# Kernel optimization log

Measured on AMD Instinct MI355X. Metric: run time of the kernel, lower is better.

## Reference

```python
import jax, jax.numpy as jnp
import numpy as np

MARGIN = 0.5


def _pairwise_sqdist(a, b):
    # ||a_i - b_j||^2 = |a_i|^2 + |b_j|^2 - 2 a_i . b_j  -> [N, N]
    a2 = jnp.sum(a * a, axis=1)
    b2 = jnp.sum(b * b, axis=1)
    return a2[:, None] + b2[None, :] - 2.0 * (a @ b.T)


def setup_inputs() -> dict:
    key = jax.random.key(0)
    k1, k2 = jax.random.split(key)
    N, D = 4096, 256
    pair1 = jax.random.normal(k1, (N, D), dtype=jnp.float32)
    pair2 = jax.random.normal(k2, (N, D), dtype=jnp.float32)
    return {"pair1": pair1, "pair2": pair2}


def reference(pair1, pair2):
    N = pair1.shape[0]
    d11 = _pairwise_sqdist(pair1, pair1)          # dist(p1_i, p1_j)
    d12 = _pairwise_sqdist(pair1, pair2)          # dist(p1_i, p2_j)
    dist_ap = jnp.diagonal(d12)                   # ||p1_i - p2_i||^2, [N]
    off_diag = 1.0 - jnp.eye(N, dtype=pair1.dtype)  # exclude j == i
    hinge = (jax.nn.relu(dist_ap[:, None] - d11 + MARGIN)
             + jax.nn.relu(dist_ap[:, None] - d12 + MARGIN))
    losses = jnp.sum(hinge * off_diag)
    cnt = N * (N - 1)
    return losses / cnt
```

## Files before the change

### kernel.cpp

```cpp
#include <hip/hip_runtime.h>

#define NN 4096
#define DD 256
#define MARGIN 0.5f

typedef __attribute__((ext_vector_type(8))) short bf16x8;
typedef __attribute__((ext_vector_type(4))) float f32x4;

__device__ inline unsigned short f32_to_bf16_rne(float v) {
    unsigned int b = __float_as_uint(v);
    b += 0x7FFFu + ((b >> 16) & 1u);
    return (unsigned short)(b >> 16);
}

__global__ __launch_bounds__(256) void stats_convert(
    const float* __restrict__ p1, const float* __restrict__ p2,
    unsigned short* __restrict__ pb, float* __restrict__ nb,
    float* __restrict__ ai)
{
    const int wave = threadIdx.x >> 6;
    const int lane = threadIdx.x & 63;
    const int row  = blockIdx.x * 4 + wave;

    const float4 x = *(const float4*)&p1[(size_t)row * DD + lane * 4];
    const float4 y = *(const float4*)&p2[(size_t)row * DD + lane * 4];

    ushort4 xb, yb;
    xb.x = f32_to_bf16_rne(x.x); xb.y = f32_to_bf16_rne(x.y);
    xb.z = f32_to_bf16_rne(x.z); xb.w = f32_to_bf16_rne(x.w);
    yb.x = f32_to_bf16_rne(y.x); yb.y = f32_to_bf16_rne(y.y);
    yb.z = f32_to_bf16_rne(y.z); yb.w = f32_to_bf16_rne(y.w);
    *(ushort4*)&pb[(size_t)row * DD + lane * 4] = xb;
    *(ushort4*)&pb[(size_t)(NN + row) * DD + lane * 4] = yb;

    float s1 = x.x*x.x + x.y*x.y + x.z*x.z + x.w*x.w;
    float s2 = y.x*y.x + y.y*y.y + y.z*y.z + y.w*y.w;
    float dx = x.x-y.x, dy = x.y-y.y, dz = x.z-y.z, dw = x.w-y.w;
    float sa = dx*dx + dy*dy + dz*dz + dw*dw;

    #pragma unroll
    for (int off = 32; off > 0; off >>= 1) {
        s1 += __shfl_down(s1, off);
        s2 += __shfl_down(s2, off);
        sa += __shfl_down(sa, off);
    }
    if (lane == 0) {
        nb[row]      = s1;
        nb[NN + row] = s2;
        ai[row]      = sa - s1 + MARGIN;
    }
}

__global__ __launch_bounds__(256, 2) void gemm_hinge(
    const unsigned short* __restrict__ pb,
    const float* __restrict__ nb, const float* __restrict__ ai,
    float* __restrict__ partial)
{
    __shared__ unsigned short Bs[2][64 * 256];
    __shared__ float wsum[4];

    const int t    = threadIdx.x;
    const int lane = t & 63;
    const int wave = t >> 6;
    const int wm   = wave >> 1;
    const int wn   = wave & 1;

    const int bid     = blockIdx.x;
    const int istripe = (bid & 7) * 4 + (bid >> 7);
    const int jgroup  = (bid >> 3) & 15;
    const int i0      = istripe * 128;

    const int lr = lane & 15;
    const int l4 = lane >> 4;
    const int lk = l4 * 8;

    bf16x8 a[4][8];
    #pragma unroll
    for (int m = 0; m < 4; ++m) {
        const unsigned short* ar = pb + (size_t)(i0 + wm * 64 + m * 16 + lr) * DD;
        #pragma unroll
        for (int kq = 0; kq < 8; ++kq)
            a[m][kq] = *(const bf16x8*)(ar + kq * 32 + lk);
    }

    const int r0 = l4 * 4;
    float aiv[4][4];
    #pragma unroll
    for (int m = 0; m < 4; ++m)
        #pragma unroll
        for (int r = 0; r < 4; ++r)
            aiv[m][r] = ai[i0 + wm * 64 + m * 16 + r0 + r];

    auto stage = [&](int sel, int jt) {
        const unsigned short* base = pb + (size_t)jt * 64 * DD;
        #pragma unroll
        for (int q = 0; q < 8; ++q) {
            const int c   = q * 256 + t;
            const int row = c >> 5;
            const int cw  = c & 31;
            const unsigned short* g = base + row * DD + ((cw ^ (row & 7)) * 8);
            __builtin_amdgcn_global_load_lds(
                (const __attribute__((address_space(1))) unsigned int*)g,
                (__attribute__((address_space(3))) unsigned int*)
                    &Bs[sel][(q * 256 + wave * 64) * 8],
                16, 0, 0);
        }
    };

    const int jt0 = jgroup * 8;
    float lsum = 0.f;

    stage(0, jt0);
    __syncthreads();

    int sel = 0;
    for (int jj = 0; jj < 8; ++jj) {
        const int j0 = (jt0 + jj) * 64;
        if (jj < 7) stage(sel ^ 1, jt0 + jj + 1);

        f32x4 acc[4][2];
        #pragma unroll
        for (int m = 0; m < 4; ++m)
            #pragma unroll
            for (int n = 0; n < 2; ++n)
                acc[m][n] = (f32x4){0.f, 0.f, 0.f, 0.f};

        #pragma unroll
        for (int kq = 0; kq < 8; ++kq) {
            bf16x8 b[2];
            #pragma unroll
            for (int n = 0; n < 2; ++n) {
                const int row = wn * 32 + n * 16 + lr;
                const int cl  = kq * 4 + l4;
                b[n] = *(const bf16x8*)&Bs[sel][row * 256 + ((cl ^ (row & 7)) * 8)];
            }
            #pragma unroll
            for (int m = 0; m < 4; ++m)
                #pragma unroll
                for (int n = 0; n < 2; ++n)
                    acc[m][n] = __builtin_amdgcn_mfma_f32_16x16x32_bf16(
                        a[m][kq], b[n], acc[m][n], 0, 0, 0);
        }

        #pragma unroll
        for (int n = 0; n < 2; ++n) {
            const int j     = j0 + wn * 32 + n * 16 + lr;
            const float nbj = nb[j];
            #pragma unroll
            for (int m = 0; m < 4; ++m) {
                #pragma unroll
                for (int r = 0; r < 4; ++r) {
                    const int i = i0 + wm * 64 + m * 16 + r0 + r;
                    float h = fmaf(2.f, acc[m][n][r], aiv[m][r] - nbj);
                    h = fmaxf(h, 0.f);
                    if (j != i && j != i + NN) lsum += h;
                }
            }
        }

        __syncthreads();
        sel ^= 1;
    }

    #pragma unroll
    for (int off = 32; off > 0; off >>= 1) lsum += __shfl_down(lsum, off);
    if (lane == 0) wsum[wave] = lsum;
    __syncthreads();
    if (t == 0)
        partial[bid] = wsum[0] + wsum[1] + wsum[2] + wsum[3];
}

__global__ __launch_bounds__(256) void final_reduce(
    const float* __restrict__ partial, float* __restrict__ out,
    int n, float scale)
{
    const int t = threadIdx.x;
    float s = 0.f;
    for (int i = t; i < n; i += 256) s += partial[i];
    #pragma unroll
    for (int off = 32; off > 0; off >>= 1) s += __shfl_down(s, off);
    __shared__ float w[4];
    if ((t & 63) == 0) w[t >> 6] = s;
    __syncthreads();
    if (t == 0) out[0] = (w[0] + w[1] + w[2] + w[3]) * scale;
}

extern "C" void kernel_launch(void* const* d_in, const int* in_sizes, int n_in,
                              void* d_out, int out_size, void* d_ws, size_t ws_size,
                              hipStream_t stream) {
    const float* p1 = (const float*)d_in[0];
    const float* p2 = (const float*)d_in[1];
    float* out = (float*)d_out;

    char* ws = (char*)d_ws;
    unsigned short* pb = (unsigned short*)ws;
    float* nb      = (float*)(ws + (size_t)2 * NN * DD * 2);
    float* ai      = nb + 2 * NN;
    float* partial = ai + NN;

    stats_convert<<<NN / 4, 256, 0, stream>>>(p1, p2, pb, nb, ai);
    gemm_hinge<<<512, 256, 0, stream>>>(pb, nb, ai, partial);
    const float scale = 1.0f / ((float)NN * (float)(NN - 1));
    final_reduce<<<1, 256, 0, stream>>>(partial, out, 512, scale);
}
```

Baseline: 36.41 us.

## Use 32x32 MFMA tiles, subtract diagonal via precomputed correction, fuse final reduce

Switches the GEMM inner loop from 16x16x32 to 32x32x16 bf16 MFMA, which halves the LDS B-fragment reads per MFMA. The per-element diagonal mask is removed from the hinge epilogue; instead stats_convert computes each row's diagonal hinge terms from the bf16-rounded values, and these are subtracted at the end. The separate final_reduce launch is replaced by a last-block-done atomic counter inside gemm_hinge. The block-to-tile mapping is also changed. Risks are small mismatches between the bf16 correction terms and the values the MFMA actually computes, plus the extra fence/atomic cost.

Measured after the change: 49.57 us. 36.1% more time.

```diff
diff --git a/kernel.cpp b/kernel.cpp
--- a/kernel.cpp
+++ b/kernel.cpp
@@ -5,19 +5,25 @@
 #define MARGIN 0.5f
 
 typedef __attribute__((ext_vector_type(8))) short bf16x8;
-typedef __attribute__((ext_vector_type(4))) float f32x4;
+typedef __attribute__((ext_vector_type(16))) float f32x16;
 
 __device__ inline unsigned short f32_to_bf16_rne(float v) {
     unsigned int b = __float_as_uint(v);
     b += 0x7FFFu + ((b >> 16) & 1u);
     return (unsigned short)(b >> 16);
 }
+__device__ inline float bf16_to_f32(unsigned short u) {
+    return __uint_as_float(((unsigned int)u) << 16);
+}
 
 __global__ __launch_bounds__(256) void stats_convert(
     const float* __restrict__ p1, const float* __restrict__ p2,
     unsigned short* __restrict__ pb, float* __restrict__ nb,
-    float* __restrict__ ai)
+    float* __restrict__ ai, float* __restrict__ corr,
+    unsigned int* __restrict__ ctr)
 {
+    if (blockIdx.x == 0 && threadIdx.x == 0) *ctr = 0u;
+
     const int wave = threadIdx.x >> 6;
     const int lane = threadIdx.x & 63;
     const int row  = blockIdx.x * 4 + wave;
@@ -38,26 +44,40 @@
     float dx = x.x-y.x, dy = x.y-y.y, dz = x.z-y.z, dw = x.w-y.w;
     float sa = dx*dx + dy*dy + dz*dz + dw*dw;
 
+    float xf0 = bf16_to_f32(xb.x), xf1 = bf16_to_f32(xb.y),
+          xf2 = bf16_to_f32(xb.z), xf3 = bf16_to_f32(xb.w);
+    float yf0 = bf16_to_f32(yb.x), yf1 = bf16_to_f32(yb.y),
+          yf2 = bf16_to_f32(yb.z), yf3 = bf16_to_f32(yb.w);
+    float s1b  = xf0*xf0 + xf1*xf1 + xf2*xf2 + xf3*xf3;
+    float s12b = xf0*yf0 + xf1*yf1 + xf2*yf2 + xf3*yf3;
+
     #pragma unroll
     for (int off = 32; off > 0; off >>= 1) {
-        s1 += __shfl_down(s1, off);
-        s2 += __shfl_down(s2, off);
-        sa += __shfl_down(sa, off);
+        s1  += __shfl_down(s1,  off);
+        s2  += __shfl_down(s2,  off);
+        sa  += __shfl_down(sa,  off);
+        s1b += __shfl_down(s1b, off);
+        s12b+= __shfl_down(s12b,off);
     }
     if (lane == 0) {
         nb[row]      = s1;
         nb[NN + row] = s2;
         ai[row]      = sa - s1 + MARGIN;
+        const float t1 = fmaxf(sa - 2.f*s1 + MARGIN + 2.f*s1b, 0.f);
+        const float t2 = fmaxf(sa - s1 - s2 + MARGIN + 2.f*s12b, 0.f);
+        corr[row] = t1 + t2;
     }
 }
 
 __global__ __launch_bounds__(256, 2) void gemm_hinge(
     const unsigned short* __restrict__ pb,
     const float* __restrict__ nb, const float* __restrict__ ai,
-    float* __restrict__ partial)
+    const float* __restrict__ corr, float* __restrict__ partial,
+    unsigned int* __restrict__ ctr, float* __restrict__ out, float scale)
 {
     __shared__ unsigned short Bs[2][64 * 256];
     __shared__ float wsum[4];
+    __shared__ int is_last;
 
     const int t    = threadIdx.x;
     const int lane = t & 63;
@@ -66,30 +86,30 @@
     const int wn   = wave & 1;
 
     const int bid     = blockIdx.x;
-    const int istripe = (bid & 7) * 4 + (bid >> 7);
-    const int jgroup  = (bid >> 3) & 15;
+    const int istripe = (bid >> 3) & 31;
+    const int jgroup  = (bid & 7) * 2 + (bid >> 8);
     const int i0      = istripe * 128;
 
-    const int lr = lane & 15;
-    const int l4 = lane >> 4;
-    const int lk = l4 * 8;
-
-    bf16x8 a[4][8];
-    #pragma unroll
-    for (int m = 0; m < 4; ++m) {
-        const unsigned short* ar = pb + (size_t)(i0 + wm * 64 + m * 16 + lr) * DD;
-        #pragma unroll
-        for (int kq = 0; kq < 8; ++kq)
-            a[m][kq] = *(const bf16x8*)(ar + kq * 32 + lk);
-    }
-
-    const int r0 = l4 * 4;
-    float aiv[4][4];
-    #pragma unroll
-    for (int m = 0; m < 4; ++m)
-        #pragma unroll
-        for (int r = 0; r < 4; ++r)
-            aiv[m][r] = ai[i0 + wm * 64 + m * 16 + r0 + r];
+    const int rA = lane & 31;
+    const int kh = lane >> 5;
+
+    bf16x8 a[2][16];
+    #pragma unroll
+    for (int m = 0; m < 2; ++m) {
+        const unsigned short* ar =
+            pb + (size_t)(i0 + wm * 64 + m * 32 + rA) * DD + kh * 8;
+        #pragma unroll
+        for (int ks = 0; ks < 16; ++ks)
+            a[m][ks] = *(const bf16x8*)(ar + ks * 16);
+    }
+
+    float aiv[2][16];
+    #pragma unroll
+    for (int m = 0; m < 2; ++m)
+        #pragma unroll
+        for (int reg = 0; reg < 16; ++reg)
+            aiv[m][reg] = ai[i0 + wm * 64 + m * 32 +
+                             (reg & 3) + 8 * (reg >> 2) + 4 * kh];
 
     auto stage = [&](int sel, int jt) {
         const unsigned short* base = pb + (size_t)jt * 64 * DD;
@@ -113,49 +133,30 @@
     stage(0, jt0);
     __syncthreads();
 
+    const int brow = wn * 32 + rA;
     int sel = 0;
     for (int jj = 0; jj < 8; ++jj) {
         const int j0 = (jt0 + jj) * 64;
         if (jj < 7) stage(sel ^ 1, jt0 + jj + 1);
 
-        f32x4 acc[4][2];
-        #pragma unroll
-        for (int m = 0; m < 4; ++m)
-            #pragma unroll
-            for (int n = 0; n < 2; ++n)
-                acc[m][n] = (f32x4){0.f, 0.f, 0.f, 0.f};
-
-        #pragma unroll
-        for (int kq = 0; kq < 8; ++kq) {
-            bf16x8 b[2];
-            #pragma unroll
-            for (int n = 0; n < 2; ++n) {
-                const int row = wn * 32 + n * 16 + lr;
-                const int cl  = kq * 4 + l4;
-                b[n] = *(const bf16x8*)&Bs[sel][row * 256 + ((cl ^ (row & 7)) * 8)];
-            }
-            #pragma unroll
-            for (int m = 0; m < 4; ++m)
-                #pragma unroll
-                for (int n = 0; n < 2; ++n)
-                    acc[m][n] = __builtin_amdgcn_mfma_f32_16x16x32_bf16(
-                        a[m][kq], b[n], acc[m][n], 0, 0, 0);
+        f32x16 acc0, acc1;
+        #pragma unroll
+        for (int q = 0; q < 16; ++q) { acc0[q] = 0.f; acc1[q] = 0.f; }
+
+        #pragma unroll
+        for (int ks = 0; ks < 16; ++ks) {
+            const int cl = ks * 2 + kh;
+            const bf16x8 b = *(const bf16x8*)
+                &Bs[sel][brow * 256 + ((cl ^ (brow & 7)) * 8)];
+            acc0 = __builtin_amdgcn_mfma_f32_32x32x16_bf16(a[0][ks], b, acc0, 0, 0, 0);
+            acc1 = __builtin_amdgcn_mfma_f32_32x32x16_bf16(a[1][ks], b, acc1, 0, 0, 0);
         }
 
-        #pragma unroll
-        for (int n = 0; n < 2; ++n) {
-            const int j     = j0 + wn * 32 + n * 16 + lr;
-            const float nbj = nb[j];
-            #pragma unroll
-            for (int m = 0; m < 4; ++m) {
-                #pragma unroll
-                for (int r = 0; r < 4; ++r) {
-                    const int i = i0 + wm * 64 + m * 16 + r0 + r;
-                    float h = fmaf(2.f, acc[m][n][r], aiv[m][r] - nbj);
-                    h = fmaxf(h, 0.f);
-                    if (j != i && j != i + NN) lsum += h;
-                }
-            }
+        const float nbj = nb[j0 + brow];
+        #pragma unroll
+        for (int reg = 0; reg < 16; ++reg) {
+            lsum += fmaxf(fmaf(2.f, acc0[reg], aiv[0][reg] - nbj), 0.f)
+                  + fmaxf(fmaf(2.f, acc1[reg], aiv[1][reg] - nbj), 0.f);
         }
 
         __syncthreads();
@@ -166,23 +167,26 @@
     for (int off = 32; off > 0; off >>= 1) lsum += __shfl_down(lsum, off);
     if (lane == 0) wsum[wave] = lsum;
     __syncthreads();
-    if (t == 0)
+    if (t == 0) {
         partial[bid] = wsum[0] + wsum[1] + wsum[2] + wsum[3];
-}
-
-__global__ __launch_bounds__(256) void final_reduce(
-    const float* __restrict__ partial, float* __restrict__ out,
-    int n, float scale)
-{
-    const int t = threadIdx.x;
-    float s = 0.f;
-    for (int i = t; i < n; i += 256) s += partial[i];
-    #pragma unroll
-    for (int off = 32; off > 0; off >>= 1) s += __shfl_down(s, off);
-    __shared__ float w[4];
-    if ((t & 63) == 0) w[t >> 6] = s;
+        __threadfence();
+        unsigned int prev = atomicAdd(ctr, 1u);
+        is_last = (prev == 511u);
+    }
     __syncthreads();
-    if (t == 0) out[0] = (w[0] + w[1] + w[2] + w[3]) * scale;
+
+    if (is_last) {
+        __threadfence();
+        float s = 0.f;
+        for (int i = t; i < 512; i += 256) s += partial[i];
+        for (int i = t; i < NN; i += 256) s -= corr[i];
+        #pragma unroll
+        for (int off = 32; off > 0; off >>= 1) s += __shfl_down(s, off);
+        if (lane == 0) wsum[wave] = s;
+        __syncthreads();
+        if (t == 0)
+            out[0] = (wsum[0] + wsum[1] + wsum[2] + wsum[3]) * scale;
+    }
 }
 
 extern "C" void kernel_launch(void* const* d_in, const int* in_sizes, int n_in,
@@ -196,10 +200,11 @@
     unsigned short* pb = (unsigned short*)ws;
     float* nb      = (float*)(ws + (size_t)2 * NN * DD * 2);
     float* ai      = nb + 2 * NN;
-    float* partial = ai + NN;
-
-    stats_convert<<<NN / 4, 256, 0, stream>>>(p1, p2, pb, nb, ai);
-    gemm_hinge<<<512, 256, 0, stream>>>(pb, nb, ai, partial);
+    float* corr    = ai + NN;
+    float* partial = corr + NN;
+    unsigned int* ctr = (unsigned int*)(partial + 512);
     const float scale = 1.0f / ((float)NN * (float)(NN - 1));
-    final_reduce<<<1, 256, 0, stream>>>(partial, out, 512, scale);
-}
+
+    stats_convert<<<NN / 4, 256, 0, stream>>>(p1, p2, pb, nb, ai, corr, ctr);
+    gemm_hinge<<<512, 256, 0, stream>>>(pb, nb, ai, corr, partial, ctr, out, scale);
+}
```
